# Kernel optimization log

Measured on AMD Instinct MI355X. Metric: run time of the kernel, lower is better.

Reference implementation:

```python
import jax, jax.numpy as jnp
import numpy as np

DIM = 768
NUM_HEADS = 12
HEAD_DIM = DIM // NUM_HEADS
SCALE = HEAD_DIM ** -0.5


def setup_inputs() -> dict:
    key = jax.random.key(0)
    ks = jax.random.split(key, 7)
    B, N, C = 8, 1024, DIM
    x = jax.random.normal(ks[0], (B, N, C), dtype=jnp.float32)
    mask = jax.random.randint(ks[1], (B, N), 0, 2) > 0  # True = masked out
    qkv_w = jax.random.normal(ks[2], (3 * C, C), dtype=jnp.float32) * 0.02
    q_bias = jax.random.normal(ks[3], (C,), dtype=jnp.float32) * 0.02
    v_bias = jax.random.normal(ks[4], (C,), dtype=jnp.float32) * 0.02
    proj_w = jax.random.normal(ks[5], (C, C), dtype=jnp.float32) * 0.02
    proj_b = jax.random.normal(ks[6], (C,), dtype=jnp.float32) * 0.02
    return {"x": x, "mask": mask, "qkv_w": qkv_w, "q_bias": q_bias,
            "v_bias": v_bias, "proj_w": proj_w, "proj_b": proj_b}


def reference(x, mask, qkv_w, q_bias, v_bias, proj_w, proj_b):
    B, N, C = x.shape
    # CAE bias: concat(q_bias, zeros, v_bias) for the fused qkv projection
    qkv_bias = jnp.concatenate([q_bias, jnp.zeros_like(v_bias), v_bias])
    qkv = x @ qkv_w.T + qkv_bias  # [B, N, 3C]
    qkv = qkv.reshape(B, N, 3, NUM_HEADS, HEAD_DIM)
    q, k, v = (qkv[:, :, i].transpose(0, 2, 1, 3) for i in range(3))  # [B,H,N,hd]
    attn = jnp.einsum('bhqd,bhkd->bhqk', q * SCALE, k)  # [B,H,N,N]
    attn = jnp.where(mask[:, None, None, :], -jnp.inf, attn)
    attn = jax.nn.softmax(attn, axis=-1)
    out = jnp.einsum('bhqk,bhkd->bhqd', attn, v)  # [B,H,N,hd]
    out = out.transpose(0, 2, 1, 3).reshape(B, N, C)
    return out @ proj_w.T + proj_b
```

## Files before the change

### kernel.cpp

```cpp
#include <hip/hip_runtime.h>
#include <cstddef>
#include <cstdint>


typedef __attribute__((ext_vector_type(4))) float f32x4;
typedef __attribute__((ext_vector_type(8))) __bf16 bf16x8;
typedef __attribute__((ext_vector_type(4))) unsigned int uint4v;
typedef __attribute__((ext_vector_type(2))) unsigned int uint2v;

#define QK_PRESCALE 0.18033688011112042f

__device__ __forceinline__ unsigned short f2bf(float f) {
  return (unsigned short)((__float_as_uint(f) + 0x8000u) >> 16);
}
__device__ __forceinline__ unsigned int pack2bf(float flo, float fhi) {
  unsigned ulo = __float_as_uint(flo) + 0x8000u;
  unsigned uhi = __float_as_uint(fhi) + 0x8000u;
  return __builtin_amdgcn_perm(uhi, ulo, 0x07060302);
}

__device__ __forceinline__ void gl_lds16(const unsigned short* g, unsigned short* l) {
  __builtin_amdgcn_global_load_lds(
      (const __attribute__((address_space(1))) unsigned int*)g,
      (__attribute__((address_space(3))) unsigned int*)l, 16, 0, 0);
}

__global__ __launch_bounds__(256)
void cvt3_kernel(const float* __restrict__ s0, unsigned short* __restrict__ d0,
                 const float* __restrict__ s1, unsigned short* __restrict__ d1,
                 const float* __restrict__ s2, unsigned short* __restrict__ d2) {
  int bid = blockIdx.x;
  const float* s; unsigned short* d; int i; int n4;
  if (bid < 6144)      { s = s0; d = d0; i = bid * 256 + threadIdx.x;            n4 = 1572864; }
  else if (bid < 7872) { s = s1; d = d1; i = (bid - 6144) * 256 + threadIdx.x;   n4 = 442368; }
  else                 { s = s2; d = d2; i = (bid - 7872) * 256 + threadIdx.x;   n4 = 147456; }
  if (i < n4) {
    float4 v = ((const float4*)s)[i];
    uint2v o;
    o.x = pack2bf(v.x, v.y);
    o.y = pack2bf(v.z, v.w);
    ((uint2v*)d)[i] = o;
  }
}

__global__ __launch_bounds__(256, 3)
void qkv_gemm(const unsigned short* __restrict__ xb, const unsigned short* __restrict__ wb,
              const float* __restrict__ qb, const float* __restrict__ vb,
              unsigned short* __restrict__ qo, unsigned short* __restrict__ ko,
              unsigned short* __restrict__ vto) {
  __shared__ __align__(16) unsigned short lds[20480];
  const int tid = threadIdx.x;
  const int lane = tid & 63, wid = tid >> 6;
  const int widu = __builtin_amdgcn_readfirstlane(wid);
  const int lm = lane & 15, lq = lane >> 4;
  const int xsw = lm & 7;
  const int wr = widu >> 1, wc = widu & 1;
  const int L = blockIdx.x;
  const int xcd = L & 7, s = L >> 3;
  const int ft = s >> 3;
  const int tt = xcd * 8 + (s & 7);
  const int m0 = tt * 128;
  const int n0 = ft * 192;
  const int srow = lane >> 3;
  const int scolsw = ((lane & 7) ^ srow) * 8;
  const unsigned short* paS = wb + (size_t)(n0 + widu * 48 + srow) * 768 + scolsw;
  const unsigned short* pbS = xb + (size_t)(m0 + widu * 32 + srow) * 768 + scolsw;
  unsigned short* const ldsA = &lds[(widu * 48) * 64];
  unsigned short* const ldsB = &lds[12288 + (widu * 32) * 64];

  f32x4 acc[6][4] = {};

  for (int t = 0; t < 12; ++t) {
    const size_t c = (size_t)t * 64;
#pragma unroll
    for (int i = 0; i < 6; ++i)
      gl_lds16(paS + (size_t)i * 8 * 768 + c, ldsA + i * 8 * 64);
#pragma unroll
    for (int i = 0; i < 4; ++i)
      gl_lds16(pbS + (size_t)i * 8 * 768 + c, ldsB + i * 8 * 64);
    __syncthreads();

    bf16x8 bff[4][2], af[3][2];
#pragma unroll
    for (int n2 = 0; n2 < 4; ++n2)
#pragma unroll
      for (int kx = 0; kx < 2; ++kx)
        bff[n2][kx] = *(const bf16x8*)&lds[12288 + (wc * 64 + n2 * 16 + lm) * 64 + (((kx * 4 + lq) ^ xsw) * 8)];
#pragma unroll
    for (int m2 = 0; m2 < 3; ++m2)
#pragma unroll
      for (int kx = 0; kx < 2; ++kx)
        af[m2][kx] = *(const bf16x8*)&lds[(wr * 96 + m2 * 16 + lm) * 64 + (((kx * 4 + lq) ^ xsw) * 8)];

    __builtin_amdgcn_s_setprio(1);
#pragma unroll
    for (int kx = 0; kx < 2; ++kx)
#pragma unroll
      for (int m2 = 0; m2 < 3; ++m2)
#pragma unroll
        for (int n2 = 0; n2 < 4; ++n2)
          acc[m2][n2] = __builtin_amdgcn_mfma_f32_16x16x32_bf16(af[m2][kx], bff[n2][kx], acc[m2][n2], 0, 0, 0);
    __builtin_amdgcn_s_setprio(0);

    bf16x8 af2[3][2];
#pragma unroll
    for (int m2 = 0; m2 < 3; ++m2)
#pragma unroll
      for (int kx = 0; kx < 2; ++kx)
        af2[m2][kx] = *(const bf16x8*)&lds[(wr * 96 + (3 + m2) * 16 + lm) * 64 + (((kx * 4 + lq) ^ xsw) * 8)];
    __builtin_amdgcn_s_setprio(1);
#pragma unroll
    for (int kx = 0; kx < 2; ++kx)
#pragma unroll
      for (int m2 = 0; m2 < 3; ++m2)
#pragma unroll
        for (int n2 = 0; n2 < 4; ++n2)
          acc[3 + m2][n2] = __builtin_amdgcn_mfma_f32_16x16x32_bf16(af2[m2][kx], bff[n2][kx], acc[3 + m2][n2], 0, 0, 0);
    __builtin_amdgcn_s_setprio(0);

    __syncthreads();
  }

  const int bq = tt >> 3;
  const int tokb = (tt & 7) * 128;
  if (n0 < 1536) {
    const bool isq = n0 < 768;
    unsigned short* dst0 = isq ? qo : ko;
#pragma unroll
    for (int mi = 0; mi < 6; ++mi) {
      const int fblk = n0 + wr * 96 + mi * 16;
      const int fd = fblk - (isq ? 0 : 768);
      const int hh = fd >> 6;
      const int dih = (fd & 63) + lq * 4;
      f32x4 bias4 = {0.f, 0.f, 0.f, 0.f};
      if (isq) bias4 = *(const f32x4*)&qb[fblk + lq * 4];
#pragma unroll
      for (int ni = 0; ni < 4; ++ni) {
        const int tok = tokb + wc * 64 + ni * 16 + lm;
        uint2v pk;
        if (isq) {
          pk.x = pack2bf((acc[mi][ni][0] + bias4[0]) * QK_PRESCALE,
                         (acc[mi][ni][1] + bias4[1]) * QK_PRESCALE);
          pk.y = pack2bf((acc[mi][ni][2] + bias4[2]) * QK_PRESCALE,
                         (acc[mi][ni][3] + bias4[3]) * QK_PRESCALE);
        } else {
          pk.x = pack2bf(acc[mi][ni][0], acc[mi][ni][1]);
          pk.y = pack2bf(acc[mi][ni][2], acc[mi][ni][3]);
        }
        *(uint2v*)&dst0[(((size_t)(bq * 12 + hh)) * 1024 + tok) * 64 + dih] = pk;
      }
    }
  } else {
    const int vb0 = n0 - 1536;
#pragma unroll
    for (int p = 0; p < 2; ++p) {
      __syncthreads();
      if (wr == p) {
#pragma unroll
        for (int mi = 0; mi < 6; ++mi) {
          f32x4 bias4 = *(const f32x4*)&vb[vb0 + p * 96 + mi * 16 + lq * 4];
#pragma unroll
          for (int ni = 0; ni < 4; ++ni) {
            const int tokl = wc * 64 + ni * 16 + lm;
#pragma unroll
            for (int r = 0; r < 4; ++r)
              lds[(mi * 16 + lq * 4 + r) * 136 + tokl] = f2bf(acc[mi][ni][r] + bias4[r]);
          }
        }
      }
      __syncthreads();
      for (int r = tid >> 1; r < 96; r += 128) {
        const int tq = tid & 1;
        const int dgv = vb0 + p * 96 + r;
        const int hh = dgv >> 6, d = dgv & 63;
        unsigned short* dstv = vto + (((size_t)(bq * 12 + hh)) * 64 + d) * 1024 + tokb + tq * 64;
        const unsigned short* srcr = &lds[r * 136 + tq * 64];
#pragma unroll
        for (int j = 0; j < 8; ++j)
          *(uint4v*)&dstv[j * 8] = *(const uint4v*)&srcr[j * 8];
      }
    }
  }
}

__global__ __launch_bounds__(256, 4)
void attn_mfma(const unsigned short* __restrict__ q, const unsigned short* __restrict__ k,
               const unsigned short* __restrict__ vt, const int* __restrict__ mask,
               unsigned short* __restrict__ ao) {
  __shared__ unsigned short ks_s[2][64 * 64];
  __shared__ unsigned short vs_s[2][64 * 64];
  __shared__ float mkl[1024];
  const int tid = threadIdx.x;
  const int lane = tid & 63, wid = tid >> 6;
  const int lm = lane & 15, lq = lane >> 4;
  const int xsw = lm & 7;
  const int plq = ((lq & 1) << 1) | (lq >> 1);
  const int L = blockIdx.x;
  const int xcd = L & 7, s = L >> 3;
  const int bh = xcd * 12 + s / 8;
  const int qt = s % 8;
  const int bb = bh / 12, hh = bh % 12;
  const unsigned short* qp = q + (size_t)bh * 65536;
  const unsigned short* kp = k + (size_t)bh * 65536;
  const unsigned short* vp = vt + (size_t)bh * 65536;
  const int* mp = mask + bb * 1024;
  const int q0 = qt * 128 + wid * 32;
  const int srow = lane >> 3;
  const int scolsw = ((lane & 7) ^ srow) * 8;
  const unsigned short* gk = kp + (size_t)(wid * 16 + srow) * 64 + scolsw;
  const unsigned short* gv = vp + (size_t)(wid * 16 + srow) * 1024 + scolsw;

#define STAGE_T(kt_, b_) { \
    gl_lds16(gk + (size_t)(kt_) * 4096, &ks_s[b_][(wid * 16) * 64]); \
    gl_lds16(gk + (size_t)(kt_) * 4096 + (size_t)8 * 64, &ks_s[b_][(wid * 16 + 8) * 64]); \
    gl_lds16(gv + (size_t)(kt_) * 64, &vs_s[b_][(wid * 16) * 64]); \
    gl_lds16(gv + (size_t)(kt_) * 64 + (size_t)8 * 1024, &vs_s[b_][(wid * 16 + 8) * 64]); }

  {
    int4 mv = ((const int4*)mp)[tid];
    float4 f;
    f.x = mv.x ? -1e30f : 0.0f;
    f.y = mv.y ? -1e30f : 0.0f;
    f.z = mv.z ? -1e30f : 0.0f;
    f.w = mv.w ? -1e30f : 0.0f;
    ((float4*)mkl)[tid] = f;
  }

  bf16x8 qf[2][2];
#pragma unroll
  for (int mi = 0; mi < 2; ++mi)
#pragma unroll
    for (int ks2 = 0; ks2 < 2; ++ks2)
      qf[mi][ks2] = *(const bf16x8*)&qp[(size_t)(q0 + mi * 16 + lm) * 64 + ks2 * 32 + lq * 8];
  bf16x8 ones;
#pragma unroll
  for (int i = 0; i < 8; ++i) ones[i] = (__bf16)1.0f;

  f32x4 o_acc[2][4] = {};
  f32x4 l_acc[2] = {};

  STAGE_T(0, 0);
  __syncthreads();

  for (int kt = 0; kt < 16; ++kt) {
    const int b = kt & 1;
    if (kt) {
      asm volatile("s_waitcnt vmcnt(0)\ns_barrier" ::: "memory");
    }
    if (kt < 15) STAGE_T(kt + 1, b ^ 1);

    f32x4 st[4][2] = {};
#pragma unroll
    for (int ks2 = 0; ks2 < 2; ++ks2) {
      bf16x8 kf[4];
#pragma unroll
      for (int nt = 0; nt < 4; ++nt)
        kf[nt] = *(const bf16x8*)&ks_s[b][(nt * 16 + lm) * 64 + (((ks2 * 4 + lq) ^ xsw) * 8)];
      __builtin_amdgcn_s_setprio(1);
#pragma unroll
      for (int nt = 0; nt < 4; ++nt)
#pragma unroll
        for (int mi = 0; mi < 2; ++mi)
          st[nt][mi] = __builtin_amdgcn_mfma_f32_16x16x32_bf16(kf[nt], qf[mi][ks2], st[nt][mi], 0, 0, 0);
      __builtin_amdgcn_s_setprio(0);
    }

#pragma unroll
    for (int h2 = 0; h2 < 2; ++h2) {
      bf16x8 pf[2];
#pragma unroll
      for (int mi = 0; mi < 2; ++mi) {
        const int ntA = h2 * 2, ntB = h2 * 2 + 1;
        f32x4 mvA = *(const f32x4*)&mkl[kt * 64 + ntA * 16 + lq * 4];
        f32x4 mvB = *(const f32x4*)&mkl[kt * 64 + ntB * 16 + lq * 4];
        unsigned a0 = pack2bf(__builtin_amdgcn_exp2f(st[ntA][mi][0] + mvA[0]),
                              __builtin_amdgcn_exp2f(st[ntA][mi][1] + mvA[1]));
        unsigned a1 = pack2bf(__builtin_amdgcn_exp2f(st[ntA][mi][2] + mvA[2]),
                              __builtin_amdgcn_exp2f(st[ntA][mi][3] + mvA[3]));
        unsigned b0 = pack2bf(__builtin_amdgcn_exp2f(st[ntB][mi][0] + mvB[0]),
                              __builtin_amdgcn_exp2f(st[ntB][mi][1] + mvB[1]));
        unsigned b1 = pack2bf(__builtin_amdgcn_exp2f(st[ntB][mi][2] + mvB[2]),
                              __builtin_amdgcn_exp2f(st[ntB][mi][3] + mvB[3]));
        asm volatile("v_permlane16_swap_b32 %0, %1" : "+v"(a0), "+v"(b0));
        asm volatile("v_permlane16_swap_b32 %0, %1" : "+v"(a1), "+v"(b1));
        uint4v u; u.x = a0; u.y = a1; u.z = b0; u.w = b1;
        pf[mi] = __builtin_bit_cast(bf16x8, u);
      }
      bf16x8 vf[4];
#pragma unroll
      for (int nt = 0; nt < 4; ++nt)
        vf[nt] = *(const bf16x8*)&vs_s[b][(nt * 16 + lm) * 64 + (((h2 * 4 + plq) ^ xsw) * 8)];
      __builtin_amdgcn_s_setprio(1);
#pragma unroll
      for (int mi = 0; mi < 2; ++mi) {
#pragma unroll
        for (int nt = 0; nt < 4; ++nt)
          o_acc[mi][nt] = __builtin_amdgcn_mfma_f32_16x16x32_bf16(pf[mi], vf[nt], o_acc[mi][nt], 0, 0, 0);
        l_acc[mi] = __builtin_amdgcn_mfma_f32_16x16x32_bf16(pf[mi], ones, l_acc[mi], 0, 0, 0);
      }
      __builtin_amdgcn_s_setprio(0);
    }
  }
#undef STAGE_T

#pragma unroll
  for (int mi = 0; mi < 2; ++mi) {
#pragma unroll
    for (int r = 0; r < 4; ++r) {
      float inv = 1.0f / l_acc[mi][r];
      int tok = q0 + mi * 16 + lq * 4 + r;
#pragma unroll
      for (int nt = 0; nt < 4; ++nt)
        ao[(size_t)(bb * 1024 + tok) * 768 + hh * 64 + nt * 16 + lm] = f2bf(o_acc[mi][nt][r] * inv);
    }
  }
}

__global__ __launch_bounds__(256, 2)
void proj_gemm(const unsigned short* __restrict__ ab, const unsigned short* __restrict__ wb,
               const float* __restrict__ pb, float* __restrict__ out) {
  __shared__ __align__(16) unsigned short lds[14336];
  const int tid = threadIdx.x;
  const int lane = tid & 63, wid = tid >> 6;
  const int widu = __builtin_amdgcn_readfirstlane(wid);
  const int lm = lane & 15, lq = lane >> 4;
  const int xsw = lm & 7;
  const int wr = widu >> 1, wc = widu & 1;
  const int L = blockIdx.x;
  const int xcd = L & 7, s = L >> 3;
  const int n0 = (s >> 3) * 96;
  const int m0 = (xcd * 8 + (s & 7)) * 128;
  const int srow = lane >> 3;
  const int scolsw = ((lane & 7) ^ srow) * 8;
  const unsigned short* paS = wb + (size_t)(n0 + widu * 24 + srow) * 768 + scolsw;
  const unsigned short* pbS = ab + (size_t)(m0 + widu * 32 + srow) * 768 + scolsw;
  unsigned short* const ldsA = &lds[(widu * 24) * 64];
  unsigned short* const ldsB = &lds[6144 + (widu * 32) * 64];

  f32x4 acc[3][4] = {};

  for (int t = 0; t < 12; ++t) {
    const size_t c = (size_t)t * 64;
#pragma unroll
    for (int i = 0; i < 3; ++i)
      gl_lds16(paS + (size_t)i * 8 * 768 + c, ldsA + i * 8 * 64);
#pragma unroll
    for (int i = 0; i < 4; ++i)
      gl_lds16(pbS + (size_t)i * 8 * 768 + c, ldsB + i * 8 * 64);
    __syncthreads();

    bf16x8 af[3][2], bff[4][2];
#pragma unroll
    for (int m2 = 0; m2 < 3; ++m2)
#pragma unroll
      for (int kx = 0; kx < 2; ++kx)
        af[m2][kx] = *(const bf16x8*)&lds[(wr * 48 + m2 * 16 + lm) * 64 + (((kx * 4 + lq) ^ xsw) * 8)];
#pragma unroll
    for (int n2 = 0; n2 < 4; ++n2)
#pragma unroll
      for (int kx = 0; kx < 2; ++kx)
        bff[n2][kx] = *(const bf16x8*)&lds[6144 + (wc * 64 + n2 * 16 + lm) * 64 + (((kx * 4 + lq) ^ xsw) * 8)];

    __builtin_amdgcn_s_setprio(1);
#pragma unroll
    for (int kx = 0; kx < 2; ++kx)
#pragma unroll
      for (int m2 = 0; m2 < 3; ++m2)
#pragma unroll
        for (int n2 = 0; n2 < 4; ++n2)
          acc[m2][n2] = __builtin_amdgcn_mfma_f32_16x16x32_bf16(af[m2][kx], bff[n2][kx], acc[m2][n2], 0, 0, 0);
    __builtin_amdgcn_s_setprio(0);

    __syncthreads();
  }

#pragma unroll
  for (int mi = 0; mi < 3; ++mi) {
    int gn0 = n0 + wr * 48 + mi * 16 + lq * 4;
    f32x4 bias4 = *(const f32x4*)&pb[gn0];
#pragma unroll
    for (int ni = 0; ni < 4; ++ni) {
      int gm = m0 + wc * 64 + ni * 16 + lm;
      f32x4 o;
      o[0] = acc[mi][ni][0] + bias4[0];
      o[1] = acc[mi][ni][1] + bias4[1];
      o[2] = acc[mi][ni][2] + bias4[2];
      o[3] = acc[mi][ni][3] + bias4[3];
      *(f32x4*)&out[(size_t)gm * 768 + gn0] = o;
    }
  }
}

extern "C" void kernel_launch(void* const* d_in, const int* in_sizes, int n_in,
                              void* d_out, int out_size, void* d_ws, size_t ws_size,
                              hipStream_t stream) {
  const float* x      = (const float*)d_in[0];
  const int*   mask   = (const int*)d_in[1];
  const float* qkv_w  = (const float*)d_in[2];
  const float* q_bias = (const float*)d_in[3];
  const float* v_bias = (const float*)d_in[4];
  const float* proj_w = (const float*)d_in[5];
  const float* proj_b = (const float*)d_in[6];
  float* out = (float*)d_out;
  unsigned short* p = (unsigned short*)d_ws;
  unsigned short* xb     = p;              p += 6291456;
  unsigned short* wqkvb  = p;              p += 1769472;
  unsigned short* wprojb = p;              p += 589824;
  unsigned short* qo     = p;              p += 6291456;
  unsigned short* ko     = p;              p += 6291456;
  unsigned short* vto    = p;              p += 6291456;
  unsigned short* ao     = p;

  cvt3_kernel<<<8448, 256, 0, stream>>>(x, xb, qkv_w, wqkvb, proj_w, wprojb);
  qkv_gemm<<<768, 256, 0, stream>>>(xb, wqkvb, q_bias, v_bias, qo, ko, vto);
  attn_mfma<<<768, 256, 0, stream>>>(qo, ko, vto, mask, ao);
  proj_gemm<<<512, 256, 0, stream>>>(ao, wprojb, proj_b, out);
}
```

Baseline: 179.7 us.

## Compact unmasked keys/values and skip fully-masked key tiles in attention

The mask conversion kernel now also computes a prefix-sum compaction of unmasked token indices per batch. A new gather kernel copies unmasked K rows and V^T columns into compacted buffers, and the attention kernel loops only over the key tiles that hold valid tokens, masking the tail by count. With a random mask about half the keys are dropped, roughly halving attention work. The cost is an extra launch plus a gather kernel that uses scalar 2-byte loads with poor coalescing over only 96 blocks.

```diff
diff --git a/kernel.cpp b/kernel.cpp
--- a/kernel.cpp
+++ b/kernel.cpp
@@ -28,8 +28,34 @@
 __global__ __launch_bounds__(256)
 void cvt3_kernel(const float* __restrict__ s0, unsigned short* __restrict__ d0,
                  const float* __restrict__ s1, unsigned short* __restrict__ d1,
-                 const float* __restrict__ s2, unsigned short* __restrict__ d2) {
+                 const float* __restrict__ s2, unsigned short* __restrict__ d2,
+                 const int* __restrict__ mask, int* __restrict__ idxA,
+                 int* __restrict__ nkA) {
+  __shared__ int sc[256];
   int bid = blockIdx.x;
+  if (bid >= 8448) {
+    const int b = bid - 8448;
+    const int t = threadIdx.x;
+    int4 mv = ((const int4*)(mask + b * 1024))[t];
+    int c = (mv.x == 0) + (mv.y == 0) + (mv.z == 0) + (mv.w == 0);
+    sc[t] = c;
+    __syncthreads();
+    for (int off = 1; off < 256; off <<= 1) {
+      int v = (t >= off) ? sc[t - off] : 0;
+      __syncthreads();
+      sc[t] += v;
+      __syncthreads();
+    }
+    int run = sc[t] - c;
+#pragma unroll
+    for (int i = 0; i < 4; ++i) {
+      int tok = t * 4 + i;
+      int m = (i == 0) ? mv.x : (i == 1) ? mv.y : (i == 2) ? mv.z : mv.w;
+      if (!m) { idxA[b * 1024 + run] = tok; run++; }
+    }
+    if (t == 0) nkA[b] = sc[255];
+    return;
+  }
   const float* s; unsigned short* d; int i; int n4;
   if (bid < 6144)      { s = s0; d = d0; i = bid * 256 + threadIdx.x;            n4 = 1572864; }
   else if (bid < 7872) { s = s1; d = d1; i = (bid - 6144) * 256 + threadIdx.x;   n4 = 442368; }
@@ -183,9 +209,43 @@
   }
 }
 
+__global__ __launch_bounds__(1024)
+void gather_kv(const unsigned short* __restrict__ ko, const unsigned short* __restrict__ vto,
+               const int* __restrict__ idxA, const int* __restrict__ nkA,
+               unsigned short* __restrict__ kc, unsigned short* __restrict__ vtc) {
+  __shared__ int idxL[1024];
+  const int bh = blockIdx.x;
+  const int b = bh / 12;
+  const int t = threadIdx.x;
+  const int nk = nkA[b];
+  if (t < 256)
+    ((int4*)idxL)[t] = ((const int4*)(idxA + b * 1024))[t];
+  __syncthreads();
+  const int w = t >> 6, lane = t & 63;
+  const unsigned short* kin = ko + (size_t)bh * 65536;
+  unsigned short* kout = kc + (size_t)bh * 65536;
+  for (int j = w; j < 1024; j += 16) {
+    int src = idxL[j] & 1023;
+    unsigned short v = kin[(size_t)src * 64 + lane];
+    kout[(size_t)j * 64 + lane] = (j < nk) ? v : (unsigned short)0;
+  }
+  const unsigned short* vin = vto + (size_t)bh * 65536;
+  unsigned short* vout = vtc + (size_t)bh * 65536;
+  for (int d = w; d < 64; d += 16) {
+    const unsigned short* vr = vin + (size_t)d * 1024;
+    unsigned short* vo = vout + (size_t)d * 1024;
+    for (int c0 = 0; c0 < 1024; c0 += 64) {
+      int j = c0 + lane;
+      int src = idxL[j] & 1023;
+      unsigned short v = vr[src];
+      vo[j] = (j < nk) ? v : (unsigned short)0;
+    }
+  }
+}
+
 __global__ __launch_bounds__(256, 4)
-void attn_mfma(const unsigned short* __restrict__ q, const unsigned short* __restrict__ k,
-               const unsigned short* __restrict__ vt, const int* __restrict__ mask,
+void attn_mfma(const unsigned short* __restrict__ q, const unsigned short* __restrict__ kcp,
+               const unsigned short* __restrict__ vtc, const int* __restrict__ nkA,
                unsigned short* __restrict__ ao) {
   __shared__ unsigned short ks_s[2][64 * 64];
   __shared__ unsigned short vs_s[2][64 * 64];
@@ -201,9 +261,11 @@
   const int qt = s % 8;
   const int bb = bh / 12, hh = bh % 12;
   const unsigned short* qp = q + (size_t)bh * 65536;
-  const unsigned short* kp = k + (size_t)bh * 65536;
-  const unsigned short* vp = vt + (size_t)bh * 65536;
-  const int* mp = mask + bb * 1024;
+  const unsigned short* kp = kcp + (size_t)bh * 65536;
+  const unsigned short* vp = vtc + (size_t)bh * 65536;
+  const int nk = nkA[bb];
+  int nkt = (nk + 63) >> 6;
+  if (nkt < 1) nkt = 1;
   const int q0 = qt * 128 + wid * 32;
   const int srow = lane >> 3;
   const int scolsw = ((lane & 7) ^ srow) * 8;
@@ -217,12 +279,12 @@
     gl_lds16(gv + (size_t)(kt_) * 64 + (size_t)8 * 1024, &vs_s[b_][(wid * 16 + 8) * 64]); }
 
   {
-    int4 mv = ((const int4*)mp)[tid];
+    int j4 = tid * 4;
     float4 f;
-    f.x = mv.x ? -1e30f : 0.0f;
-    f.y = mv.y ? -1e30f : 0.0f;
-    f.z = mv.z ? -1e30f : 0.0f;
-    f.w = mv.w ? -1e30f : 0.0f;
+    f.x = (j4 + 0 < nk) ? 0.0f : -1e30f;
+    f.y = (j4 + 1 < nk) ? 0.0f : -1e30f;
+    f.z = (j4 + 2 < nk) ? 0.0f : -1e30f;
+    f.w = (j4 + 3 < nk) ? 0.0f : -1e30f;
     ((float4*)mkl)[tid] = f;
   }
 
@@ -242,12 +304,12 @@
   STAGE_T(0, 0);
   __syncthreads();
 
-  for (int kt = 0; kt < 16; ++kt) {
+  for (int kt = 0; kt < nkt; ++kt) {
     const int b = kt & 1;
     if (kt) {
       asm volatile("s_waitcnt vmcnt(0)\ns_barrier" ::: "memory");
     }
-    if (kt < 15) STAGE_T(kt + 1, b ^ 1);
+    if (kt + 1 < nkt) STAGE_T(kt + 1, b ^ 1);
 
     f32x4 st[4][2] = {};
 #pragma unroll
@@ -409,10 +471,16 @@
   unsigned short* qo     = p;              p += 6291456;
   unsigned short* ko     = p;              p += 6291456;
   unsigned short* vto    = p;              p += 6291456;
-  unsigned short* ao     = p;
-
-  cvt3_kernel<<<8448, 256, 0, stream>>>(x, xb, qkv_w, wqkvb, proj_w, wprojb);
+  unsigned short* ao     = p;              p += 6291456;
+  unsigned short* kc     = p;              p += 6291456;
+  unsigned short* vtc    = p;              p += 6291456;
+  int* idxA = (int*)p;
+  int* nkA  = idxA + 8192;
+
+  cvt3_kernel<<<8456, 256, 0, stream>>>(x, xb, qkv_w, wqkvb, proj_w, wprojb,
+                                        mask, idxA, nkA);
   qkv_gemm<<<768, 256, 0, stream>>>(xb, wqkvb, q_bias, v_bias, qo, ko, vto);
-  attn_mfma<<<768, 256, 0, stream>>>(qo, ko, vto, mask, ao);
+  gather_kv<<<96, 1024, 0, stream>>>(ko, vto, idxA, nkA, kc, vtc);
+  attn_mfma<<<768, 256, 0, stream>>>(qo, kc, vtc, nkA, ao);
   proj_gemm<<<512, 256, 0, stream>>>(ao, wprojb, proj_b, out);
 }
```

Result: no change. 179.8 us (+0.0%).
